# Kernel optimization log

Measured on AMD Instinct MI355X. Metric: run time of the kernel, lower is better.

## Reference

```python
import jax, jax.numpy as jnp
import numpy as np

B, CQ, CKV, H, W = 8, 256, 512, 64, 64
HKV, WKV = 32, 32
DQK = CQ // 8  # 32


def setup_inputs() -> dict:
    key = jax.random.key(0)
    ks = jax.random.split(key, 9)
    s = 0.05
    return {
        "query": jax.random.normal(ks[0], (B, CQ, H, W), jnp.float32),
        "key_value": jax.random.normal(ks[1], (B, CKV, HKV, WKV), jnp.float32),
        "Wq": jax.random.normal(ks[2], (DQK, CQ), jnp.float32) * s,
        "bq": jax.random.normal(ks[3], (DQK,), jnp.float32) * s,
        "Wk": jax.random.normal(ks[4], (DQK, CKV), jnp.float32) * s,
        "bk": jax.random.normal(ks[5], (DQK,), jnp.float32) * s,
        "Wv": jax.random.normal(ks[6], (CQ, CKV), jnp.float32) * s,
        "bv": jax.random.normal(ks[7], (CQ,), jnp.float32) * s,
        "gamma": jax.random.normal(ks[8], (1,), jnp.float32) * 0.5,
    }


def reference(query, key_value, Wq, bq, Wk, bk, Wv, bv, gamma):
    b, cq, h, w = query.shape
    n = h * w
    # bilinear resize of key_value to query's spatial size (align_corners=False
    # half-pixel convention, matching torch F.interpolate and jax.image.resize)
    kv = jax.image.resize(key_value, (b, key_value.shape[1], h, w), method="bilinear")
    # 1x1 convs are channel contractions
    q = jnp.einsum("bchw,dc->bdhw", query, Wq) + bq[None, :, None, None]   # [B,DQK,H,W]
    k = jnp.einsum("bchw,dc->bdhw", kv, Wk) + bk[None, :, None, None]      # [B,DQK,H,W]
    v = jnp.einsum("bchw,dc->bdhw", kv, Wv) + bv[None, :, None, None]      # [B,CQ,H,W]
    qf = q.reshape(b, -1, n)   # [B,DQK,N]
    kf = k.reshape(b, -1, n)   # [B,DQK,N]
    vf = v.reshape(b, -1, n)   # [B,CQ,N]
    energy = jnp.einsum("bdn,bdm->bnm", qf, kf)        # [B,N,N]
    attention = jax.nn.softmax(energy, axis=-1)
    out = jnp.einsum("bnm,bcm->bcn", attention, vf)     # [B,CQ,N]
    out = out.reshape(b, cq, h, w)
    return gamma[0] * out + query
```

## Files before the change

kernel.cpp:

```cpp
#include <hip/hip_runtime.h>

#define B_ 8
#define CQ_ 256
#define CKV_ 512
#define N_ 4096
#define DQK_ 32
#define LOG2E 1.44269504f

typedef __bf16 bf16;
typedef __bf16 bf16x4 __attribute__((ext_vector_type(4)));
typedef __bf16 bf16x8 __attribute__((ext_vector_type(8)));
typedef float f32x4 __attribute__((ext_vector_type(4)));

__global__ void k_convert_w(const float* __restrict__ Wq, const float* __restrict__ Wk,
                            const float* __restrict__ Wv,
                            bf16* __restrict__ wq, bf16* __restrict__ wk, bf16* __restrict__ wv) {
    int i = blockIdx.x * 256 + threadIdx.x;
    if (i < 8192) wq[i] = (bf16)(Wq[i] * LOG2E);
    else if (i < 24576) wk[i - 8192] = (bf16)Wk[i - 8192];
    else if (i < 155648) wv[i - 24576] = (bf16)Wv[i - 24576];
}

__global__ __launch_bounds__(256) void k_resize(const float* __restrict__ kv, bf16* __restrict__ kvr) {
    const int yo = blockIdx.x;
    const int b  = blockIdx.y;
    const int uc = blockIdx.z * 64;
    const int tid = threadIdx.x;
    __shared__ float r0[64][33];
    __shared__ float r1[64][33];
    int ty = yo >> 1;
    int y0, y1; float wy0, wy1;
    if ((yo & 1) == 0) { y0 = ty > 0 ? ty - 1 : 0; y1 = ty; wy0 = 0.25f; wy1 = 0.75f; }
    else               { y0 = ty; y1 = ty < 31 ? ty + 1 : 31; wy0 = 0.75f; wy1 = 0.25f; }
    const int u_loc = tid & 63;
    const int xo_base = tid >> 6;
    for (int i = 0; i < 8; ++i) {
        int idx = tid + i * 256;
        int u = idx >> 5, x = idx & 31;
        const float* src = kv + ((size_t)b * CKV_ + uc + u) * 1024 + x;
        r0[u][x] = src[y0 * 32];
        r1[u][x] = src[y1 * 32];
    }
    __syncthreads();
    for (int i = 0; i < 16; ++i) {
        int xo = xo_base + i * 4;
        int tx = xo >> 1;
        int xa, xb; float wxa, wxb;
        if ((xo & 1) == 0) { xa = tx > 0 ? tx - 1 : 0; xb = tx; wxa = 0.25f; wxb = 0.75f; }
        else               { xa = tx; xb = tx < 31 ? tx + 1 : 31; wxa = 0.75f; wxb = 0.25f; }
        float v0 = wxa * r0[u_loc][xa] + wxb * r0[u_loc][xb];
        float v1 = wxa * r1[u_loc][xa] + wxb * r1[u_loc][xb];
        float val = wy0 * v0 + wy1 * v1;
        kvr[((size_t)b * N_ + yo * 64 + xo) * CKV_ + uc + u_loc] = (bf16)val;
    }
}

__global__ __launch_bounds__(256) void k_proj_q_fused(const float* __restrict__ query,
                                                      const bf16* __restrict__ W,
                                                      const float* __restrict__ bias,
                                                      bf16* __restrict__ qTb) {
    __shared__ bf16 tile[64][264];
    const int n0 = blockIdx.x * 64;
    const int b  = blockIdx.y;
    const int tid = threadIdx.x;
    const int xi = tid & 15, c0 = tid >> 4;
    for (int pass = 0; pass < 16; ++pass) {
        int c = c0 + pass * 16;
        const float4 v = *(const float4*)(query + ((size_t)b * CQ_ + c) * N_ + n0 + xi * 4);
        tile[xi * 4 + 0][c] = (bf16)v.x;
        tile[xi * 4 + 1][c] = (bf16)v.y;
        tile[xi * 4 + 2][c] = (bf16)v.z;
        tile[xi * 4 + 3][c] = (bf16)v.w;
    }
    __syncthreads();
    const int w = tid >> 6, lane = tid & 63;
    const int l16 = lane & 15, quad = lane >> 4;
    const int ct = w & 1, nh = w >> 1;
    f32x4 acc[2];
    acc[0] = (f32x4){0.f, 0.f, 0.f, 0.f}; acc[1] = (f32x4){0.f, 0.f, 0.f, 0.f};
    const bf16* aptr = W + (ct * 16 + l16) * CQ_ + quad * 8;
#pragma unroll
    for (int ks = 0; ks < 8; ++ks) {
        bf16x8 af = *(const bf16x8*)(aptr + ks * 32);
        for (int j = 0; j < 2; ++j) {
            bf16x8 bfv = *(const bf16x8*)&tile[nh * 32 + j * 16 + l16][ks * 32 + quad * 8];
            acc[j] = __builtin_amdgcn_mfma_f32_16x16x32_bf16(af, bfv, acc[j], 0, 0, 0);
        }
    }
    for (int j = 0; j < 2; ++j)
        for (int r = 0; r < 4; ++r) {
            int d = ct * 16 + quad * 4 + r;
            int n = n0 + nh * 32 + j * 16 + l16;
            qTb[((size_t)b * N_ + n) * DQK_ + d] = (bf16)(acc[j][r] + bias[d] * LOG2E);
        }
}

__global__ __launch_bounds__(256) void k_proj_k(const bf16* __restrict__ W,
                                                const float* __restrict__ bias,
                                                const bf16* __restrict__ Bm,
                                                bf16* __restrict__ outT) {
    const int flat = blockIdx.x + 128 * blockIdx.y;
    const int b  = flat & 7;
    const int mb = (flat >> 3) * 32;
    const int tid = threadIdx.x;
    const int w = tid >> 6, lane = tid & 63;
    const int l16 = lane & 15, quad = lane >> 4;
    const int ct = w & 1;
    const int mh = (w >> 1) * 16;
    f32x4 acc = (f32x4){0.f, 0.f, 0.f, 0.f};
    const bf16* aptr = W + (ct * 16 + l16) * CKV_ + quad * 8;
    const bf16* bptr = Bm + ((size_t)b * N_ + mb + mh + l16) * CKV_ + quad * 8;
#pragma unroll
    for (int ks = 0; ks < 16; ++ks) {
        bf16x8 af  = *(const bf16x8*)(aptr + ks * 32);
        bf16x8 bfv = *(const bf16x8*)(bptr + ks * 32);
        acc = __builtin_amdgcn_mfma_f32_16x16x32_bf16(af, bfv, acc, 0, 0, 0);
    }
    const int m = mb + mh + l16;
    for (int r = 0; r < 4; ++r) {
        int d = ct * 16 + quad * 4 + r;
        outT[((size_t)b * N_ + m) * DQK_ + d] = (bf16)(acc[r] + bias[d]);
    }
}

__global__ __launch_bounds__(256) void k_proj_v(const bf16* __restrict__ W,
                                                const float* __restrict__ bias,
                                                const bf16* __restrict__ Bm,
                                                bf16* __restrict__ vout) {
    const int flat = blockIdx.x + 128 * blockIdx.y;
    const int b  = flat & 7;
    const int mb = (flat >> 3) * 32;
    const int tid = threadIdx.x;
    const int w = tid >> 6, lane = tid & 63;
    const int l16 = lane & 15, quad = lane >> 4;
    f32x4 acc[4][2];
    for (int i = 0; i < 4; ++i) for (int j = 0; j < 2; ++j) acc[i][j] = (f32x4){0.f, 0.f, 0.f, 0.f};
    const bf16* bbase = Bm + ((size_t)b * N_ + mb) * CKV_ + quad * 8;
#pragma unroll 4
    for (int ks = 0; ks < 16; ++ks) {
        bf16x8 bfv[2];
        for (int j = 0; j < 2; ++j)
            bfv[j] = *(const bf16x8*)(bbase + (size_t)(j * 16 + l16) * CKV_ + ks * 32);
        for (int i = 0; i < 4; ++i) {
            bf16x8 af = *(const bf16x8*)(W + (size_t)((w * 4 + i) * 16 + l16) * CKV_ + ks * 32 + quad * 8);
            for (int j = 0; j < 2; ++j)
                acc[i][j] = __builtin_amdgcn_mfma_f32_16x16x32_bf16(af, bfv[j], acc[i][j], 0, 0, 0);
        }
    }
    for (int i = 0; i < 4; ++i)
        for (int r = 0; r < 4; ++r) {
            int c = (w * 4 + i) * 16 + quad * 4 + r;
            float bvs = bias[c];
            for (int j = 0; j < 2; ++j) {
                int m = mb + j * 16 + l16;
                vout[((size_t)b * CQ_ + c) * N_ + m] = (bf16)(acc[i][j][r] + bvs);
            }
        }
}

__global__ __launch_bounds__(256, 4) void k_flash(const bf16* __restrict__ qT,
                                                  const bf16* __restrict__ kT,
                                                  const bf16* __restrict__ vv,
                                                  const float* __restrict__ query,
                                                  const float* __restrict__ gamma,
                                                  float* __restrict__ out) {
    __shared__ bf16 P[2][64][72];
    __shared__ float linvs[64];
    const int z = blockIdx.z;
    const int tid = threadIdx.x;
    const int w = tid >> 6, lane = tid & 63;
    const int l16 = lane & 15, quad = lane >> 4;
    const int swz = l16 & 3;
    const int flat = blockIdx.x + 64 * blockIdx.y;
    const int b  = flat & 7;
    const int n0 = (flat >> 3) * 64;

    const bf16x8 qfrag = *(const bf16x8*)(qT + ((size_t)b * N_ + n0 + w * 16 + l16) * DQK_ + quad * 8);

    f32x4 acc[2][4];
    for (int i = 0; i < 2; ++i) for (int j = 0; j < 4; ++j) acc[i][j] = (f32x4){0.f, 0.f, 0.f, 0.f};
    f32x4 lsum = (f32x4){0.f, 0.f, 0.f, 0.f};

    const bf16* kbase = kT + (size_t)b * N_ * DQK_;
    const bf16* vbase = vv + ((size_t)b * CQ_ + z * 128 + w * 32) * N_;

    auto loadK = [&](int mt, bf16x8* dst) {
        for (int im = 0; im < 4; ++im)
            dst[im] = *(const bf16x8*)(kbase + (size_t)(mt * 64 + im * 16 + l16) * DQK_ + quad * 8);
    };
    auto computeS = [&](const bf16x8* kfr, bf16 (*Pb)[72]) {
        for (int im = 0; im < 4; ++im) {
            f32x4 s = __builtin_amdgcn_mfma_f32_16x16x32_bf16(kfr[im], qfrag,
                                                              (f32x4){0.f, 0.f, 0.f, 0.f}, 0, 0, 0);
            bf16x4 pk;
            for (int r = 0; r < 4; ++r) {
                float p = exp2f(s[r]);
                lsum[r] += p;
                pk[r] = (bf16)p;
            }
            *(bf16x4*)&Pb[w * 16 + l16][((im ^ swz) << 4) + quad * 4] = pk;
        }
    };

    bf16x8 kf[4];
    loadK(0, kf);
    computeS(kf, P[0]);
    loadK(1, kf);
    __syncthreads();

    for (int u = 0; u < 63; ++u) {
        const int m0 = u * 64;
        bf16x8 vf[2][2];
        for (int ks = 0; ks < 2; ++ks)
            for (int i = 0; i < 2; ++i)
                vf[ks][i] = *(const bf16x8*)(vbase + (size_t)(i * 16 + l16) * N_ + m0 + ks * 32 + quad * 8);
        computeS(kf, P[(u + 1) & 1]);
        loadK(u + 2 < 64 ? u + 2 : 0, kf);
        bf16 (* __restrict__ Pb)[72] = P[u & 1];
        __builtin_amdgcn_s_setprio(1);
        for (int ks = 0; ks < 2; ++ks) {
            bf16x8 pf[4];
            for (int j = 0; j < 4; ++j)
                pf[j] = *(const bf16x8*)&Pb[j * 16 + l16]
                            [((((ks << 1) | (quad >> 1)) ^ swz) << 4) + ((quad & 1) << 3)];
            for (int i = 0; i < 2; ++i)
                for (int j = 0; j < 4; ++j)
                    acc[i][j] = __builtin_amdgcn_mfma_f32_16x16x32_bf16(vf[ks][i], pf[j], acc[i][j], 0, 0, 0);
        }
        __builtin_amdgcn_s_setprio(0);
        __syncthreads();
    }
    {
        const int m0 = 63 * 64;
        bf16x8 vf[2][2];
        for (int ks = 0; ks < 2; ++ks)
            for (int i = 0; i < 2; ++i)
                vf[ks][i] = *(const bf16x8*)(vbase + (size_t)(i * 16 + l16) * N_ + m0 + ks * 32 + quad * 8);
        bf16 (* __restrict__ Pb)[72] = P[1];
        for (int ks = 0; ks < 2; ++ks) {
            bf16x8 pf[4];
            for (int j = 0; j < 4; ++j)
                pf[j] = *(const bf16x8*)&Pb[j * 16 + l16]
                            [((((ks << 1) | (quad >> 1)) ^ swz) << 4) + ((quad & 1) << 3)];
            for (int i = 0; i < 2; ++i)
                for (int j = 0; j < 4; ++j)
                    acc[i][j] = __builtin_amdgcn_mfma_f32_16x16x32_bf16(vf[ks][i], pf[j], acc[i][j], 0, 0, 0);
        }
    }
    float s = (lsum[0] + lsum[1]) + (lsum[2] + lsum[3]);
    s += __shfl_xor(s, 16);
    s += __shfl_xor(s, 32);
    if (lane < 16) linvs[w * 16 + l16] = 1.f / s;
    __syncthreads();
    float linv[4];
    for (int j = 0; j < 4; ++j) linv[j] = linvs[j * 16 + l16];
    const float g = gamma[0];
    for (int i = 0; i < 2; ++i)
        for (int r = 0; r < 4; ++r) {
            int c = z * 128 + w * 32 + i * 16 + quad * 4 + r;
            for (int j = 0; j < 4; ++j) {
                int n = n0 + j * 16 + l16;
                size_t idx = ((size_t)b * CQ_ + c) * N_ + n;
                out[idx] = g * acc[i][j][r] * linv[j] + query[idx];
            }
        }
}

extern "C" void kernel_launch(void* const* d_in, const int* in_sizes, int n_in,
                              void* d_out, int out_size, void* d_ws, size_t ws_size,
                              hipStream_t stream) {
    const float* query     = (const float*)d_in[0];
    const float* key_value = (const float*)d_in[1];
    const float* Wq = (const float*)d_in[2];
    const float* bq = (const float*)d_in[3];
    const float* Wk = (const float*)d_in[4];
    const float* bk = (const float*)d_in[5];
    const float* Wv = (const float*)d_in[6];
    const float* bv = (const float*)d_in[7];
    const float* gamma = (const float*)d_in[8];
    float* out = (float*)d_out;

    char* ws = (char*)d_ws;
    bf16* kvr  = (bf16*)(ws);
    bf16* vbuf = (bf16*)(ws + 33554432);
    bf16* qTb  = (bf16*)(ws + 50331648);
    bf16* kTb  = (bf16*)(ws + 52428800);
    bf16* wqb  = (bf16*)(ws + 54525952);
    bf16* wkb  = (bf16*)(ws + 54542336);
    bf16* wvb  = (bf16*)(ws + 54575104);

    k_convert_w<<<608, 256, 0, stream>>>(Wq, Wk, Wv, wqb, wkb, wvb);
    k_resize<<<dim3(64, 8, 8), 256, 0, stream>>>(key_value, kvr);
    k_proj_q_fused<<<dim3(64, 8), 256, 0, stream>>>(query, wqb, bq, qTb);
    k_proj_k<<<dim3(128, 8), 256, 0, stream>>>(wkb, bk, kvr, kTb);
    k_proj_v<<<dim3(128, 8), 256, 0, stream>>>(wvb, bv, kvr, vbuf);
    k_flash<<<dim3(64, 8, 2), 256, 0, stream>>>(qTb, kTb, vbuf, query, gamma, out);
}
```

Baseline: 358.6 us.

## Make flash-attention waves independent, each owning its query rows and private P buffer

Restructures the attention kernel so each wave computes P for its own 16 query rows and multiplies by all 128 value channels. The P tile becomes per-wave in shared memory, which removes every block-level barrier and the shared reciprocal-sum exchange. V fragments are now loaded per wave for all channels and software-prefetched across iterations. In exchange each wave reads 4x more V data from global/L2 (no cross-wave reuse of V), and register pressure rises because the occupancy hint of 4 blocks per CU is dropped.

```diff
diff --git a/kernel.cpp b/kernel.cpp
--- a/kernel.cpp
+++ b/kernel.cpp
@@ -158,14 +158,13 @@
         }
 }
 
-__global__ __launch_bounds__(256, 4) void k_flash(const bf16* __restrict__ qT,
-                                                  const bf16* __restrict__ kT,
-                                                  const bf16* __restrict__ vv,
-                                                  const float* __restrict__ query,
-                                                  const float* __restrict__ gamma,
-                                                  float* __restrict__ out) {
-    __shared__ bf16 P[2][64][72];
-    __shared__ float linvs[64];
+__global__ __launch_bounds__(256) void k_flash(const bf16* __restrict__ qT,
+                                               const bf16* __restrict__ kT,
+                                               const bf16* __restrict__ vv,
+                                               const float* __restrict__ query,
+                                               const float* __restrict__ gamma,
+                                               float* __restrict__ out) {
+    __shared__ bf16 P[4][16][72];
     const int z = blockIdx.z;
     const int tid = threadIdx.x;
     const int w = tid >> 6, lane = tid & 63;
@@ -174,23 +173,40 @@
     const int flat = blockIdx.x + 64 * blockIdx.y;
     const int b  = flat & 7;
     const int n0 = (flat >> 3) * 64;
-
-    const bf16x8 qfrag = *(const bf16x8*)(qT + ((size_t)b * N_ + n0 + w * 16 + l16) * DQK_ + quad * 8);
-
-    f32x4 acc[2][4];
-    for (int i = 0; i < 2; ++i) for (int j = 0; j < 4; ++j) acc[i][j] = (f32x4){0.f, 0.f, 0.f, 0.f};
+    const int nw = n0 + w * 16;
+
+    const bf16x8 qfrag = *(const bf16x8*)(qT + ((size_t)b * N_ + nw + l16) * DQK_ + quad * 8);
+
+    f32x4 acc[8];
+#pragma unroll
+    for (int i = 0; i < 8; ++i) acc[i] = (f32x4){0.f, 0.f, 0.f, 0.f};
     f32x4 lsum = (f32x4){0.f, 0.f, 0.f, 0.f};
 
     const bf16* kbase = kT + (size_t)b * N_ * DQK_;
-    const bf16* vbase = vv + ((size_t)b * CQ_ + z * 128 + w * 32) * N_;
+    const bf16* vbase = vv + ((size_t)b * CQ_ + z * 128) * N_ + (size_t)l16 * N_ + quad * 8;
+
+    bf16 (* __restrict__ Pw)[72] = P[w];
+    const int roff0 = ((((0 << 1) | (quad >> 1)) ^ swz) << 4) + ((quad & 1) << 3);
+    const int roff1 = ((((1 << 1) | (quad >> 1)) ^ swz) << 4) + ((quad & 1) << 3);
 
     auto loadK = [&](int mt, bf16x8* dst) {
         for (int im = 0; im < 4; ++im)
             dst[im] = *(const bf16x8*)(kbase + (size_t)(mt * 64 + im * 16 + l16) * DQK_ + quad * 8);
     };
-    auto computeS = [&](const bf16x8* kfr, bf16 (*Pb)[72]) {
+    auto loadV = [&](int m0, int ks, bf16x8* dst) {
+        for (int i = 0; i < 8; ++i)
+            dst[i] = *(const bf16x8*)(vbase + (size_t)i * (16 * N_) + m0 + ks * 32);
+    };
+
+    bf16x8 kf[4];
+    loadK(0, kf);
+    bf16x8 vf0[8];
+    loadV(0, 0, vf0);
+
+    for (int u = 0; u < 64; ++u) {
+        const int m0 = u * 64;
         for (int im = 0; im < 4; ++im) {
-            f32x4 s = __builtin_amdgcn_mfma_f32_16x16x32_bf16(kfr[im], qfrag,
+            f32x4 s = __builtin_amdgcn_mfma_f32_16x16x32_bf16(kf[im], qfrag,
                                                               (f32x4){0.f, 0.f, 0.f, 0.f}, 0, 0, 0);
             bf16x4 pk;
             for (int r = 0; r < 4; ++r) {
@@ -198,71 +214,36 @@
                 lsum[r] += p;
                 pk[r] = (bf16)p;
             }
-            *(bf16x4*)&Pb[w * 16 + l16][((im ^ swz) << 4) + quad * 4] = pk;
-        }
-    };
-
-    bf16x8 kf[4];
-    loadK(0, kf);
-    computeS(kf, P[0]);
-    loadK(1, kf);
-    __syncthreads();
-
-    for (int u = 0; u < 63; ++u) {
-        const int m0 = u * 64;
-        bf16x8 vf[2][2];
-        for (int ks = 0; ks < 2; ++ks)
-            for (int i = 0; i < 2; ++i)
-                vf[ks][i] = *(const bf16x8*)(vbase + (size_t)(i * 16 + l16) * N_ + m0 + ks * 32 + quad * 8);
-        computeS(kf, P[(u + 1) & 1]);
-        loadK(u + 2 < 64 ? u + 2 : 0, kf);
-        bf16 (* __restrict__ Pb)[72] = P[u & 1];
+            *(bf16x4*)&Pw[l16][((im ^ swz) << 4) + quad * 4] = pk;
+        }
+        loadK((u + 1) & 63, kf);
+        bf16x8 vf1[8];
+        loadV(m0, 1, vf1);
+        bf16x8 pf0 = *(const bf16x8*)&Pw[l16][roff0];
         __builtin_amdgcn_s_setprio(1);
-        for (int ks = 0; ks < 2; ++ks) {
-            bf16x8 pf[4];
-            for (int j = 0; j < 4; ++j)
-                pf[j] = *(const bf16x8*)&Pb[j * 16 + l16]
-                            [((((ks << 1) | (quad >> 1)) ^ swz) << 4) + ((quad & 1) << 3)];
-            for (int i = 0; i < 2; ++i)
-                for (int j = 0; j < 4; ++j)
-                    acc[i][j] = __builtin_amdgcn_mfma_f32_16x16x32_bf16(vf[ks][i], pf[j], acc[i][j], 0, 0, 0);
-        }
+        for (int i = 0; i < 8; ++i)
+            acc[i] = __builtin_amdgcn_mfma_f32_16x16x32_bf16(vf0[i], pf0, acc[i], 0, 0, 0);
         __builtin_amdgcn_s_setprio(0);
-        __syncthreads();
-    }
-    {
-        const int m0 = 63 * 64;
-        bf16x8 vf[2][2];
-        for (int ks = 0; ks < 2; ++ks)
-            for (int i = 0; i < 2; ++i)
-                vf[ks][i] = *(const bf16x8*)(vbase + (size_t)(i * 16 + l16) * N_ + m0 + ks * 32 + quad * 8);
-        bf16 (* __restrict__ Pb)[72] = P[1];
-        for (int ks = 0; ks < 2; ++ks) {
-            bf16x8 pf[4];
-            for (int j = 0; j < 4; ++j)
-                pf[j] = *(const bf16x8*)&Pb[j * 16 + l16]
-                            [((((ks << 1) | (quad >> 1)) ^ swz) << 4) + ((quad & 1) << 3)];
-            for (int i = 0; i < 2; ++i)
-                for (int j = 0; j < 4; ++j)
-                    acc[i][j] = __builtin_amdgcn_mfma_f32_16x16x32_bf16(vf[ks][i], pf[j], acc[i][j], 0, 0, 0);
-        }
-    }
+        bf16x8 pf1 = *(const bf16x8*)&Pw[l16][roff1];
+        __builtin_amdgcn_s_setprio(1);
+        for (int i = 0; i < 8; ++i)
+            acc[i] = __builtin_amdgcn_mfma_f32_16x16x32_bf16(vf1[i], pf1, acc[i], 0, 0, 0);
+        __builtin_amdgcn_s_setprio(0);
+        loadV(((u + 1) & 63) * 64, 0, vf0);
+    }
+
     float s = (lsum[0] + lsum[1]) + (lsum[2] + lsum[3]);
     s += __shfl_xor(s, 16);
     s += __shfl_xor(s, 32);
-    if (lane < 16) linvs[w * 16 + l16] = 1.f / s;
-    __syncthreads();
-    float linv[4];
-    for (int j = 0; j < 4; ++j) linv[j] = linvs[j * 16 + l16];
+    const float linv = 1.f / s;
     const float g = gamma[0];
-    for (int i = 0; i < 2; ++i)
+    const int n = nw + l16;
+#pragma unroll
+    for (int i = 0; i < 8; ++i)
         for (int r = 0; r < 4; ++r) {
-            int c = z * 128 + w * 32 + i * 16 + quad * 4 + r;
-            for (int j = 0; j < 4; ++j) {
-                int n = n0 + j * 16 + l16;
-                size_t idx = ((size_t)b * CQ_ + c) * N_ + n;
-                out[idx] = g * acc[i][j][r] * linv[j] + query[idx];
-            }
+            int c = z * 128 + i * 16 + quad * 4 + r;
+            size_t idx = ((size_t)b * CQ_ + c) * N_ + n;
+            out[idx] = g * acc[i][r] * linv + query[idx];
         }
 }
 
```

After: 689.5 us. 1.92x slower.
